# Performance work log

Measured on AMD Instinct MI355X. Metric: run time of the kernel, lower is better.

## Reference

```python
import jax, jax.numpy as jnp
import numpy as np

N_NODES = 50000
N_EDGES = 800000
IN_CH = 128
HID = 64
HEADS = 4
OUT_CH = 64
NEG_SLOPE = 0.2


def _add_self_loops(ei, n):
    loops = jnp.tile(jnp.arange(n, dtype=ei.dtype)[None, :], (2, 1))
    return jnp.concatenate([ei, loops], axis=1)


def _gat_conv(x, ei, W, a_s, a_d, b, concat):
    """PyG-style GATConv. x:[N,F], ei:[2,E], W:[F,H*C], a_s/a_d:[H,C]."""
    N = x.shape[0]
    H, C = a_s.shape
    h = (x @ W).reshape(N, H, C)                     # [N,H,C]
    src, dst = ei[0], ei[1]
    al_s = (h * a_s[None]).sum(-1)                   # [N,H]
    al_d = (h * a_d[None]).sum(-1)                   # [N,H]
    logits = jax.nn.leaky_relu(al_s[src] + al_d[dst], NEG_SLOPE)  # [E,H]
    # segment softmax over incoming edges of each dst node
    m = jax.ops.segment_max(logits, dst, num_segments=N)
    m = jax.lax.stop_gradient(jnp.where(jnp.isfinite(m), m, 0.0))
    ex = jnp.exp(logits - m[dst])
    denom = jax.ops.segment_sum(ex, dst, num_segments=N)
    alpha = ex / (denom[dst] + 1e-16)                # [E,H]
    out = jax.ops.segment_sum(alpha[:, :, None] * h[src], dst, num_segments=N)  # [N,H,C]
    out = out.reshape(N, H * C) if concat else out.mean(axis=1)
    return out + b


def _hetero_layer(x, edges, self_loop_flags, W, a_s, a_d, b, concat):
    N = x.shape[0]
    out = None
    for r in range(3):
        ei = _add_self_loops(edges[r], N) if self_loop_flags[r] else edges[r]
        o = _gat_conv(x, ei, W[r], a_s[r], a_d[r], b[r], concat)
        out = o if out is None else out + o
    return out


def setup_inputs() -> dict:
    key = jax.random.key(0)
    ks = jax.random.split(key, 16)
    s = 0.05
    return {
        "x": jax.random.normal(ks[0], (N_NODES, IN_CH), jnp.float32),
        "e_blocks": jax.random.randint(ks[1], (2, N_EDGES), 0, N_NODES),
        "e_spatial": jax.random.randint(ks[2], (2, N_EDGES), 0, N_NODES),
        "e_similar": jax.random.randint(ks[3], (2, N_EDGES), 0, N_NODES),
        "W1": jax.random.normal(ks[4], (3, IN_CH, HEADS * HID), jnp.float32) * s,
        "a1s": jax.random.normal(ks[5], (3, HEADS, HID), jnp.float32) * s,
        "a1d": jax.random.normal(ks[6], (3, HEADS, HID), jnp.float32) * s,
        "b1": jax.random.normal(ks[7], (3, HEADS * HID), jnp.float32) * s,
        "W2": jax.random.normal(ks[8], (3, HEADS * HID, HEADS * HID), jnp.float32) * s,
        "a2s": jax.random.normal(ks[9], (3, HEADS, HID), jnp.float32) * s,
        "a2d": jax.random.normal(ks[10], (3, HEADS, HID), jnp.float32) * s,
        "b2": jax.random.normal(ks[11], (3, HID), jnp.float32) * s,
        "Wl": jax.random.normal(ks[12], (HID, OUT_CH), jnp.float32) * s,
        "bl": jax.random.normal(ks[13], (OUT_CH,), jnp.float32) * s,
    }


def reference(x, e_blocks, e_spatial, e_similar, W1, a1s, a1d, b1,
              W2, a2s, a2d, b2, Wl, bl):
    edges = [e_blocks, e_spatial, e_similar]
    self_loops = [False, True, True]  # 'blocks' has add_self_loops=False
    h = _hetero_layer(x, edges, self_loops, W1, a1s, a1d, b1, concat=True)
    h = jax.nn.relu(h)
    h = _hetero_layer(h, edges, self_loops, W2, a2s, a2d, b2, concat=False)
    h = jax.nn.relu(h)
    return h @ Wl + bl
```

## Files before the change

### kernel.cpp

```cpp
#include <hip/hip_runtime.h>
#include <hip/hip_bf16.h>
#include <hip/hip_fp16.h>

#define NN 50000
#define NE 800000
#define FIN 128
#define HCC 256
#define OC 64
#define NSL 0.2f
#define NT3 (3 * NN)

typedef __attribute__((ext_vector_type(8))) short sh8;
typedef __attribute__((ext_vector_type(16))) float f32x16;

struct __attribute__((aligned(8))) h4 { __half x, y, z, w; };
struct __attribute__((aligned(8))) s4 { short x, y, z, w; };

__device__ __forceinline__ unsigned short bf_rne(float f) {
  unsigned u = __float_as_uint(f);
  u += 0x7FFF + ((u >> 16) & 1);
  return (unsigned short)(u >> 16);
}

__device__ __forceinline__ float edge_w(float lg) {
  lg = (lg > 0.f) ? lg : NSL * lg;
  return __expf(lg);
}

template<int KK>
__global__ __launch_bounds__(256) void k_prep(const float* __restrict__ W,
                                              short* __restrict__ out) {
  int i = blockIdx.x * 256 + threadIdx.x;
  if (i >= 3 * KK * 256) return;
  int r = i / (KK * 256);
  int rem = i - r * KK * 256;
  int k = rem >> 8;
  int n = rem & 255;
  float f = W[i];
  unsigned short hb = bf_rne(f);
  float hf = __uint_as_float(((unsigned)hb) << 16);
  unsigned short lb = bf_rne(f - hf);
  int cb = n >> 7, c = n & 127, ks8 = k >> 3, kj = k & 7;
  size_t base = (size_t)r * 4 * KK * 128;
  size_t oh = base + ((size_t)((cb * 2 + 0) * (KK / 8) + ks8) * 128 + c) * 8 + kj;
  size_t ol = base + ((size_t)((cb * 2 + 1) * (KK / 8) + ks8) * 128 + c) * 8 + kj;
  out[oh] = (short)hb;
  out[ol] = (short)lb;
}

__global__ __launch_bounds__(256) void k_split(const float* __restrict__ x,
                                               short* __restrict__ xhi,
                                               short* __restrict__ xlo) {
  int i = blockIdx.x * 256 + threadIdx.x;
  if (i >= NN * FIN / 4) return;
  float4 v = ((const float4*)x)[i];
  s4 h, l;
  float f, hf;
  f = v.x; h.x = (short)bf_rne(f); hf = __uint_as_float(((unsigned)(unsigned short)h.x) << 16); l.x = (short)bf_rne(f - hf);
  f = v.y; h.y = (short)bf_rne(f); hf = __uint_as_float(((unsigned)(unsigned short)h.y) << 16); l.y = (short)bf_rne(f - hf);
  f = v.z; h.z = (short)bf_rne(f); hf = __uint_as_float(((unsigned)(unsigned short)h.z) << 16); l.z = (short)bf_rne(f - hf);
  f = v.w; h.w = (short)bf_rne(f); hf = __uint_as_float(((unsigned)(unsigned short)h.w) << 16); l.w = (short)bf_rne(f - hf);
  ((s4*)xhi)[i] = h;
  ((s4*)xlo)[i] = l;
}

__global__ void k_hist3(const int* __restrict__ e0, const int* __restrict__ e1,
                        const int* __restrict__ e2, int* __restrict__ deg3) {
  int i = blockIdx.x * blockDim.x + threadIdx.x;
  int st = gridDim.x * blockDim.x;
  for (; i < 3 * NE; i += st) {
    int rel = i / NE;
    int j = i - rel * NE;
    const int* e = (rel == 0) ? e0 : ((rel == 1) ? e1 : e2);
    atomicAdd(&deg3[rel * NN + e[NE + j]], 1);
  }
}

__global__ __launch_bounds__(1024) void k_bsum(const int* __restrict__ deg3,
                                               int* __restrict__ bsum) {
  __shared__ int s[1024];
  int t = threadIdx.x;
  int i = blockIdx.x * 1024 + t;
  s[t] = (i < NT3) ? deg3[i] : 0;
  __syncthreads();
  for (int off = 512; off > 0; off >>= 1) {
    if (t < off) s[t] += s[t + off];
    __syncthreads();
  }
  if (t == 0) bsum[blockIdx.x] = s[0];
}

__global__ __launch_bounds__(256) void k_scan2(const int* __restrict__ bsum,
                                               int* __restrict__ boffs, int nb) {
  __shared__ int s[256];
  int t = threadIdx.x;
  int v = (t < nb) ? bsum[t] : 0;
  s[t] = v;
  __syncthreads();
  for (int off = 1; off < 256; off <<= 1) {
    int x = (t >= off) ? s[t - off] : 0;
    __syncthreads();
    s[t] += x;
    __syncthreads();
  }
  if (t < nb) boffs[t] = s[t] - v;
}

__global__ __launch_bounds__(1024) void k_rowptr(const int* __restrict__ deg3,
                                                 const int* __restrict__ boffs,
                                                 int* __restrict__ rpA,
                                                 int* __restrict__ cursor3) {
  __shared__ int s[1024];
  int t = threadIdx.x;
  int i = blockIdx.x * 1024 + t;
  int d = (i < NT3) ? deg3[i] : 0;
  s[t] = d;
  __syncthreads();
  for (int off = 1; off < 1024; off <<= 1) {
    int x = (t >= off) ? s[t - off] : 0;
    __syncthreads();
    s[t] += x;
    __syncthreads();
  }
  if (i < NT3) {
    int excl = boffs[blockIdx.x] + s[t] - d;
    int r = (i < NN) ? 0 : ((i < 2 * NN) ? 1 : 2);
    int n = i - r * NN;
    int val = excl - r * NE;
    rpA[r * (NN + 1) + n] = val;
    cursor3[i] = val;
  }
  if (blockIdx.x == 0 && t < 3) rpA[t * (NN + 1) + NN] = NE;
}

__global__ void k_scatter(const int* __restrict__ srcv, const int* __restrict__ dstv,
                          int* __restrict__ cursor, int* __restrict__ csr_src, int n) {
  int i = blockIdx.x * blockDim.x + threadIdx.x;
  int st = gridDim.x * blockDim.x;
  for (; i < n; i += st) {
    int pos = atomicAdd(&cursor[dstv[i]], 1);
    csr_src[pos] = srcv[i];
  }
}

template<int KK>
__global__ __launch_bounds__(256) void k_mgemm(const short* __restrict__ Ahi,
                                               const short* __restrict__ Alo,
                                               const short* __restrict__ BcAll,
                                               const float* __restrict__ asfAll,
                                               const float* __restrict__ adfAll,
                                               __half* __restrict__ houtAll,
                                               float* __restrict__ alsAll,
                                               float* __restrict__ aldAll, int M) {
  const int rel = blockIdx.y;
  const short* Bc = BcAll + (size_t)rel * 4 * KK * 128;
  const float* asf = asfAll + rel * HCC;
  const float* adf = adfAll + rel * HCC;
  __half* hout = houtAll + (size_t)rel * NN * HCC;
  float* als = alsAll + (size_t)rel * NN * 4;
  float* ald = aldAll + (size_t)rel * NN * 4;

  const int tid = threadIdx.x;
  const int lane = tid & 63;
  const int w = tid >> 6;
  const int l31 = lane & 31;
  const int lg = lane >> 5;
  const int wrow = blockIdx.x * 64 + (w & 1) * 32;
  const int ch = w >> 1;

  f32x16 acc[4];
#pragma unroll
  for (int t = 0; t < 4; ++t) acc[t] = (f32x16)(0.f);

  const int r = wrow + l31;
  const bool aok = r < M;
  const short* ahp = Ahi + (size_t)r * KK;
  const short* alp = Alo + (size_t)r * KK;
  const short* bh = Bc + (size_t)(ch * 2 + 0) * KK * 128 + l31 * 8;
  const short* bl = Bc + (size_t)(ch * 2 + 1) * KK * 128 + l31 * 8;

  const int NK = KK / 16;

#define LOADF(kst, AH, AL, BH, BL)                                     \
  {                                                                    \
    const int k0 = (kst) * 16 + lg * 8;                                \
    AH = (sh8){0, 0, 0, 0, 0, 0, 0, 0};                                \
    AL = AH;                                                           \
    if (aok) {                                                         \
      AH = *(const sh8*)(ahp + k0);                                    \
      AL = *(const sh8*)(alp + k0);                                    \
    }                                                                  \
    const int ks8 = (kst) * 2 + lg;                                    \
    const short* bhp = bh + (size_t)ks8 * 1024;                        \
    const short* blp = bl + (size_t)ks8 * 1024;                        \
    _Pragma("unroll")                                                  \
    for (int t = 0; t < 4; ++t) {                                      \
      BH[t] = *(const sh8*)(bhp + t * 256);                            \
      BL[t] = *(const sh8*)(blp + t * 256);                            \
    }                                                                  \
  }

#define MMBLK(AH, AL, BH, BL)                                                       \
  {                                                                                 \
    _Pragma("unroll")                                                               \
    for (int t = 0; t < 4; ++t) {                                                   \
      acc[t] = __builtin_amdgcn_mfma_f32_32x32x16_bf16(AH, BH[t], acc[t], 0, 0, 0); \
      acc[t] = __builtin_amdgcn_mfma_f32_32x32x16_bf16(AL, BH[t], acc[t], 0, 0, 0); \
      acc[t] = __builtin_amdgcn_mfma_f32_32x32x16_bf16(AH, BL[t], acc[t], 0, 0, 0); \
    }                                                                               \
  }

  sh8 a0h, a0l, b0h[4], b0l[4];
  sh8 a1h, a1l, b1h[4], b1l[4];
  LOADF(0, a0h, a0l, b0h, b0l);
#pragma unroll
  for (int kst = 0; kst < NK - 1; ++kst) {
    if ((kst & 1) == 0) {
      LOADF(kst + 1, a1h, a1l, b1h, b1l);
      MMBLK(a0h, a0l, b0h, b0l);
    } else {
      LOADF(kst + 1, a0h, a0l, b0h, b0l);
      MMBLK(a1h, a1l, b1h, b1l);
    }
  }
  MMBLK(a1h, a1l, b1h, b1l);
#undef LOADF
#undef MMBLK

  float asr[4], adr[4];
#pragma unroll
  for (int t = 0; t < 4; ++t) {
    int col = ch * 128 + t * 32 + l31;
    asr[t] = asf[col];
    adr[t] = adf[col];
  }
#pragma unroll
  for (int v = 0; v < 16; ++v) {
    const int rl = (v & 3) + 8 * (v >> 2) + 4 * lg;
    const int row = wrow + rl;
    const bool rok = row < M;
    float s0 = 0.f, s1 = 0.f, d0 = 0.f, d1 = 0.f;
    __half* hp = hout + (size_t)row * 256 + ch * 128 + l31;
#pragma unroll
    for (int t = 0; t < 4; ++t) {
      float dv = acc[t][v];
      if (rok) hp[t * 32] = __float2half(dv);
      if (t < 2) { s0 += dv * asr[t]; d0 += dv * adr[t]; }
      else       { s1 += dv * asr[t]; d1 += dv * adr[t]; }
    }
#pragma unroll
    for (int m = 1; m < 32; m <<= 1) {
      s0 += __shfl_xor(s0, m);
      s1 += __shfl_xor(s1, m);
      d0 += __shfl_xor(d0, m);
      d1 += __shfl_xor(d1, m);
    }
    if (rok && l31 == 0) {
      *(float2*)(als + (size_t)row * 4 + ch * 2) = make_float2(s0, s1);
      *(float2*)(ald + (size_t)row * 4 + ch * 2) = make_float2(d0, d1);
    }
  }
}

template<bool SL>
__device__ __forceinline__ void gat_rel(int n, int head, size_t loff,
                                        const __half* __restrict__ h,
                                        const float* __restrict__ als,
                                        const float* __restrict__ ald,
                                        const int* __restrict__ rp,
                                        const int* __restrict__ cs,
                                        float& ox, float& oy, float& oz, float& ow) {
  float ad = ald[n * 4 + head];
  int rs = rp[n], re = rp[n + 1];
  float ax = 0.f, ay = 0.f, az = 0.f, aw = 0.f, wsum = 0.f;
  int i = rs;
  for (; i + 4 <= re; i += 4) {
    int s0 = cs[i], s1 = cs[i + 1], s2 = cs[i + 2], s3 = cs[i + 3];
    float al0 = als[s0 * 4 + head];
    float al1 = als[s1 * 4 + head];
    float al2 = als[s2 * 4 + head];
    float al3 = als[s3 * 4 + head];
    h4 v0 = *(const h4*)&h[(size_t)s0 * HCC + loff];
    h4 v1 = *(const h4*)&h[(size_t)s1 * HCC + loff];
    h4 v2 = *(const h4*)&h[(size_t)s2 * HCC + loff];
    h4 v3 = *(const h4*)&h[(size_t)s3 * HCC + loff];
    float w0 = edge_w(al0 + ad), w1 = edge_w(al1 + ad);
    float w2 = edge_w(al2 + ad), w3 = edge_w(al3 + ad);
    wsum += (w0 + w1) + (w2 + w3);
    ax = fmaf(w0, __half2float(v0.x), ax); ay = fmaf(w0, __half2float(v0.y), ay);
    az = fmaf(w0, __half2float(v0.z), az); aw = fmaf(w0, __half2float(v0.w), aw);
    ax = fmaf(w1, __half2float(v1.x), ax); ay = fmaf(w1, __half2float(v1.y), ay);
    az = fmaf(w1, __half2float(v1.z), az); aw = fmaf(w1, __half2float(v1.w), aw);
    ax = fmaf(w2, __half2float(v2.x), ax); ay = fmaf(w2, __half2float(v2.y), ay);
    az = fmaf(w2, __half2float(v2.z), az); aw = fmaf(w2, __half2float(v2.w), aw);
    ax = fmaf(w3, __half2float(v3.x), ax); ay = fmaf(w3, __half2float(v3.y), ay);
    az = fmaf(w3, __half2float(v3.z), az); aw = fmaf(w3, __half2float(v3.w), aw);
  }
  for (; i < re; ++i) {
    int s = cs[i];
    float w = edge_w(als[s * 4 + head] + ad);
    wsum += w;
    h4 hv = *(const h4*)&h[(size_t)s * HCC + loff];
    ax = fmaf(w, __half2float(hv.x), ax);
    ay = fmaf(w, __half2float(hv.y), ay);
    az = fmaf(w, __half2float(hv.z), az);
    aw = fmaf(w, __half2float(hv.w), aw);
  }
  if (SL) {
    float w = edge_w(als[n * 4 + head] + ad);
    wsum += w;
    h4 hv = *(const h4*)&h[(size_t)n * HCC + loff];
    ax = fmaf(w, __half2float(hv.x), ax);
    ay = fmaf(w, __half2float(hv.y), ay);
    az = fmaf(w, __half2float(hv.z), az);
    aw = fmaf(w, __half2float(hv.w), aw);
  }
  float inv = 1.0f / (wsum + 1e-16f);
  ox = fmaf(ax, inv, ox);
  oy = fmaf(ay, inv, oy);
  oz = fmaf(az, inv, oz);
  ow = fmaf(aw, inv, ow);
}

__global__ __launch_bounds__(256) void k_gather3c(const __half* __restrict__ h3,
                                                  const float* __restrict__ als3,
                                                  const float* __restrict__ ald3,
                                                  const int* __restrict__ rpA,
                                                  const int* __restrict__ csAll,
                                                  const float* __restrict__ bias,
                                                  short* __restrict__ o1hi,
                                                  short* __restrict__ o1lo) {
  int gid = blockIdx.x * blockDim.x + threadIdx.x;
  int n = gid >> 6;
  int lane = threadIdx.x & 63;
  if (n >= NN) return;
  int head = lane >> 4;
  size_t loff = (size_t)lane * 4;
  const size_t HS = (size_t)NN * HCC;
  const size_t AS = (size_t)NN * 4;
  float ox = 0.f, oy = 0.f, oz = 0.f, ow = 0.f;
  gat_rel<false>(n, head, loff, h3,          als3,          ald3,          rpA,                csAll,          ox, oy, oz, ow);
  gat_rel<true >(n, head, loff, h3 + HS,     als3 + AS,     ald3 + AS,     rpA + (NN + 1),     csAll + NE,     ox, oy, oz, ow);
  gat_rel<true >(n, head, loff, h3 + 2 * HS, als3 + 2 * AS, ald3 + 2 * AS, rpA + 2 * (NN + 1), csAll + 2 * NE, ox, oy, oz, ow);
  float4 b0 = *(const float4*)&bias[lane * 4];
  float4 b1 = *(const float4*)&bias[HCC + lane * 4];
  float4 b2 = *(const float4*)&bias[2 * HCC + lane * 4];
  float vv[4];
  vv[0] = fmaxf(ox + b0.x + b1.x + b2.x, 0.f);
  vv[1] = fmaxf(oy + b0.y + b1.y + b2.y, 0.f);
  vv[2] = fmaxf(oz + b0.z + b1.z + b2.z, 0.f);
  vv[3] = fmaxf(ow + b0.w + b1.w + b2.w, 0.f);
  s4 hv, lv;
  short* hp = (short*)&hv;
  short* lp = (short*)&lv;
#pragma unroll
  for (int j = 0; j < 4; ++j) {
    unsigned short hb = bf_rne(vv[j]);
    float hf = __uint_as_float(((unsigned)hb) << 16);
    hp[j] = (short)hb;
    lp[j] = (short)bf_rne(vv[j] - hf);
  }
  *(s4*)&o1hi[(size_t)n * HCC + loff] = hv;
  *(s4*)&o1lo[(size_t)n * HCC + loff] = lv;
}

__global__ __launch_bounds__(256) void k_gather3f(const __half* __restrict__ h3,
                                                  const float* __restrict__ als3,
                                                  const float* __restrict__ ald3,
                                                  const int* __restrict__ rpA,
                                                  const int* __restrict__ csAll,
                                                  const float* __restrict__ bias,
                                                  const float* __restrict__ Wl,
                                                  const float* __restrict__ bl,
                                                  float* __restrict__ outp) {
  __shared__ float Ws[64 * 64];
  for (int i = threadIdx.x; i < 4096; i += 256) Ws[i] = Wl[i];
  __syncthreads();
  int gid = blockIdx.x * blockDim.x + threadIdx.x;
  int n = gid >> 6;
  int lane = threadIdx.x & 63;
  if (n >= NN) return;
  int head = lane >> 4;
  size_t loff = (size_t)lane * 4;
  const size_t HS = (size_t)NN * HCC;
  const size_t AS = (size_t)NN * 4;
  float ox = 0.f, oy = 0.f, oz = 0.f, ow = 0.f;
  gat_rel<false>(n, head, loff, h3,          als3,          ald3,          rpA,                csAll,          ox, oy, oz, ow);
  gat_rel<true >(n, head, loff, h3 + HS,     als3 + AS,     ald3 + AS,     rpA + (NN + 1),     csAll + NE,     ox, oy, oz, ow);
  gat_rel<true >(n, head, loff, h3 + 2 * HS, als3 + 2 * AS, ald3 + 2 * AS, rpA + 2 * (NN + 1), csAll + 2 * NE, ox, oy, oz, ow);
  ox += __shfl_xor(ox, 16); oy += __shfl_xor(oy, 16);
  oz += __shfl_xor(oz, 16); ow += __shfl_xor(ow, 16);
  ox += __shfl_xor(ox, 32); oy += __shfl_xor(oy, 32);
  oz += __shfl_xor(oz, 32); ow += __shfl_xor(ow, 32);
  int q0 = lane & 15;
  float4 b0 = *(const float4*)&bias[q0 * 4];
  float4 b1 = *(const float4*)&bias[OC + q0 * 4];
  float4 b2 = *(const float4*)&bias[2 * OC + q0 * 4];
  float x0 = fmaxf(0.25f * ox + b0.x + b1.x + b2.x, 0.f);
  float x1 = fmaxf(0.25f * oy + b0.y + b1.y + b2.y, 0.f);
  float x2 = fmaxf(0.25f * oz + b0.z + b1.z + b2.z, 0.f);
  float x3 = fmaxf(0.25f * ow + b0.w + b1.w + b2.w, 0.f);
  float acc = bl[lane];
#pragma unroll
  for (int q = 0; q < 16; ++q) {
    float xa = __shfl(x0, q);
    float xb = __shfl(x1, q);
    float xc = __shfl(x2, q);
    float xd = __shfl(x3, q);
    acc = fmaf(xa, Ws[(4 * q + 0) * 64 + lane], acc);
    acc = fmaf(xb, Ws[(4 * q + 1) * 64 + lane], acc);
    acc = fmaf(xc, Ws[(4 * q + 2) * 64 + lane], acc);
    acc = fmaf(xd, Ws[(4 * q + 3) * 64 + lane], acc);
  }
  outp[(size_t)n * OC + lane] = acc;
}

extern "C" void kernel_launch(void* const* d_in, const int* in_sizes, int n_in,
                              void* d_out, int out_size, void* d_ws, size_t ws_size,
                              hipStream_t stream) {
  const float* x   = (const float*)d_in[0];
  const int* e_b   = (const int*)d_in[1];
  const int* e_sp  = (const int*)d_in[2];
  const int* e_si  = (const int*)d_in[3];
  const float* W1  = (const float*)d_in[4];
  const float* a1s = (const float*)d_in[5];
  const float* a1d = (const float*)d_in[6];
  const float* b1  = (const float*)d_in[7];
  const float* W2  = (const float*)d_in[8];
  const float* a2s = (const float*)d_in[9];
  const float* a2d = (const float*)d_in[10];
  const float* b2  = (const float*)d_in[11];
  const float* Wl  = (const float*)d_in[12];
  const float* bl  = (const float*)d_in[13];
  float* out = (float*)d_out;

  char* ws = (char*)d_ws;
  size_t off = 0;
  auto alloc = [&](size_t b) {
    char* p = ws + off;
    off += (b + 255) & ~(size_t)255;
    return p;
  };
  __half* h3  = (__half*)alloc((size_t)3 * NN * HCC * 2);
  short* o1hi = (short*)alloc((size_t)NN * HCC * 2);
  short* o1lo = (short*)alloc((size_t)NN * HCC * 2);
  short* xhi  = (short*)alloc((size_t)NN * FIN * 2);
  short* xlo  = (short*)alloc((size_t)NN * FIN * 2);
  float* als3 = (float*)alloc((size_t)3 * NN * 4 * 4);
  float* ald3 = (float*)alloc((size_t)3 * NN * 4 * 4);
  int* deg3    = (int*)alloc((size_t)NT3 * 4);
  int* cursor3 = (int*)alloc((size_t)NT3 * 4);
  int* rpA     = (int*)alloc((size_t)3 * (NN + 1) * 4);
  int* bsum    = (int*)alloc(256 * 4);
  int* boffs   = (int*)alloc(256 * 4);
  short* Wc1   = (short*)alloc((size_t)3 * 4 * FIN * 128 * 2);
  short* Wc2   = (short*)alloc((size_t)3 * 4 * HCC * 128 * 2);
  int* csAll   = (int*)alloc((size_t)3 * NE * 4);

  const int* edges[3] = {e_b, e_sp, e_si};

  k_prep<FIN><<<(3 * FIN * 256 + 255) / 256, 256, 0, stream>>>(W1, Wc1);
  k_prep<HCC><<<(3 * HCC * 256 + 255) / 256, 256, 0, stream>>>(W2, Wc2);
  k_split<<<(NN * FIN / 4 + 255) / 256, 256, 0, stream>>>(x, xhi, xlo);

  hipMemsetAsync(deg3, 0, (size_t)NT3 * 4, stream);
  k_hist3<<<2048, 256, 0, stream>>>(e_b, e_sp, e_si, deg3);
  const int NB = (NT3 + 1023) / 1024;
  k_bsum<<<NB, 1024, 0, stream>>>(deg3, bsum);
  k_scan2<<<1, 256, 0, stream>>>(bsum, boffs, NB);
  k_rowptr<<<NB, 1024, 0, stream>>>(deg3, boffs, rpA, cursor3);
  for (int r = 0; r < 3; ++r)
    k_scatter<<<1024, 256, 0, stream>>>(edges[r], edges[r] + NE, cursor3 + r * NN,
                                        csAll + (size_t)r * NE, NE);

  const int gblocks = (NN + 63) / 64;
  const int ablocks = (NN * 64) / 256;

  k_mgemm<FIN><<<dim3(gblocks, 3), 256, 0, stream>>>(
      xhi, xlo, Wc1, a1s, a1d, h3, als3, ald3, NN);
  k_gather3c<<<ablocks, 256, 0, stream>>>(
      h3, als3, ald3, rpA, csAll, b1, o1hi, o1lo);

  k_mgemm<HCC><<<dim3(gblocks, 3), 256, 0, stream>>>(
      o1hi, o1lo, Wc2, a2s, a2d, h3, als3, ald3, NN);
  k_gather3f<<<ablocks, 256, 0, stream>>>(
      h3, als3, ald3, rpA, csAll, b2, Wl, bl, out);
}
```

Before: 864.7 us.

## Stage weight tiles in double-buffered LDS via global_load_lds in split-bf16 GEMM

The projection GEMM now copies each k-step's weight tile into a double-buffered LDS area using direct global-to-LDS loads. Waves then read their B fragments from LDS instead of each loading them separately from global memory. The weight prep kernel reorders the packed bf16 hi/lo weights so each k-step's tile is contiguous. This cuts redundant global/L2 traffic for B, at the cost of a block-wide barrier every k-step and 32KB of LDS per block, which may lower occupancy.

```diff
diff --git a/kernel.cpp b/kernel.cpp
--- a/kernel.cpp
+++ b/kernel.cpp
@@ -15,6 +15,9 @@
 
 struct __attribute__((aligned(8))) h4 { __half x, y, z, w; };
 struct __attribute__((aligned(8))) s4 { short x, y, z, w; };
+
+typedef const __attribute__((address_space(1))) unsigned int* gas_t;
+typedef __attribute__((address_space(3))) unsigned int* las_t;
 
 __device__ __forceinline__ unsigned short bf_rne(float f) {
   unsigned u = __float_as_uint(f);
@@ -40,10 +43,11 @@
   unsigned short hb = bf_rne(f);
   float hf = __uint_as_float(((unsigned)hb) << 16);
   unsigned short lb = bf_rne(f - hf);
-  int cb = n >> 7, c = n & 127, ks8 = k >> 3, kj = k & 7;
+  int cb = n >> 7, c = n & 127;
+  int kst = k >> 4, p = (k >> 3) & 1, kj = k & 7;
   size_t base = (size_t)r * 4 * KK * 128;
-  size_t oh = base + ((size_t)((cb * 2 + 0) * (KK / 8) + ks8) * 128 + c) * 8 + kj;
-  size_t ol = base + ((size_t)((cb * 2 + 1) * (KK / 8) + ks8) * 128 + c) * 8 + kj;
+  size_t oh = base + ((size_t)(kst * 8 + (cb * 2 + 0) * 2 + p) * 128 + c) * 8 + kj;
+  size_t ol = base + ((size_t)(kst * 8 + (cb * 2 + 1) * 2 + p) * 128 + c) * 8 + kj;
   out[oh] = (short)hb;
   out[ol] = (short)lb;
 }
@@ -152,8 +156,9 @@
                                                __half* __restrict__ houtAll,
                                                float* __restrict__ alsAll,
                                                float* __restrict__ aldAll, int M) {
+  __shared__ short Bs[2][8192];
   const int rel = blockIdx.y;
-  const short* Bc = BcAll + (size_t)rel * 4 * KK * 128;
+  const short* Brel = BcAll + (size_t)rel * 4 * KK * 128;
   const float* asf = asfAll + rel * HCC;
   const float* adf = adfAll + rel * HCC;
   __half* hout = houtAll + (size_t)rel * NN * HCC;
@@ -176,55 +181,61 @@
   const bool aok = r < M;
   const short* ahp = Ahi + (size_t)r * KK;
   const short* alp = Alo + (size_t)r * KK;
-  const short* bh = Bc + (size_t)(ch * 2 + 0) * KK * 128 + l31 * 8;
-  const short* bl = Bc + (size_t)(ch * 2 + 1) * KK * 128 + l31 * 8;
+  const int qh = (ch * 2 + 0) * 2 + lg;
+  const int ql = (ch * 2 + 1) * 2 + lg;
 
   const int NK = KK / 16;
 
-#define LOADF(kst, AH, AL, BH, BL)                                     \
-  {                                                                    \
-    const int k0 = (kst) * 16 + lg * 8;                                \
-    AH = (sh8){0, 0, 0, 0, 0, 0, 0, 0};                                \
-    AL = AH;                                                           \
-    if (aok) {                                                         \
-      AH = *(const sh8*)(ahp + k0);                                    \
-      AL = *(const sh8*)(alp + k0);                                    \
-    }                                                                  \
-    const int ks8 = (kst) * 2 + lg;                                    \
-    const short* bhp = bh + (size_t)ks8 * 1024;                        \
-    const short* blp = bl + (size_t)ks8 * 1024;                        \
-    _Pragma("unroll")                                                  \
-    for (int t = 0; t < 4; ++t) {                                      \
-      BH[t] = *(const sh8*)(bhp + t * 256);                            \
-      BL[t] = *(const sh8*)(blp + t * 256);                            \
-    }                                                                  \
-  }
-
-#define MMBLK(AH, AL, BH, BL)                                                       \
-  {                                                                                 \
-    _Pragma("unroll")                                                               \
-    for (int t = 0; t < 4; ++t) {                                                   \
-      acc[t] = __builtin_amdgcn_mfma_f32_32x32x16_bf16(AH, BH[t], acc[t], 0, 0, 0); \
-      acc[t] = __builtin_amdgcn_mfma_f32_32x32x16_bf16(AL, BH[t], acc[t], 0, 0, 0); \
-      acc[t] = __builtin_amdgcn_mfma_f32_32x32x16_bf16(AH, BL[t], acc[t], 0, 0, 0); \
-    }                                                                               \
-  }
-
-  sh8 a0h, a0l, b0h[4], b0l[4];
-  sh8 a1h, a1l, b1h[4], b1l[4];
-  LOADF(0, a0h, a0l, b0h, b0l);
-#pragma unroll
-  for (int kst = 0; kst < NK - 1; ++kst) {
-    if ((kst & 1) == 0) {
-      LOADF(kst + 1, a1h, a1l, b1h, b1l);
-      MMBLK(a0h, a0l, b0h, b0l);
-    } else {
-      LOADF(kst + 1, a0h, a0l, b0h, b0l);
-      MMBLK(a1h, a1l, b1h, b1l);
+#define STAGE(kst, buf)                                                      \
+  {                                                                          \
+    _Pragma("unroll")                                                        \
+    for (int it = 0; it < 4; ++it) {                                         \
+      int so = it * 2048 + w * 512;                                          \
+      __builtin_amdgcn_global_load_lds(                                      \
+          (gas_t)(const void*)(Brel + (size_t)(kst) * 8192 + so + lane * 8), \
+          (las_t)(void*)&Bs[buf][so], 16, 0, 0);                             \
+    }                                                                        \
+  }
+
+#define LOADA(kst, AH, AL)                 \
+  {                                        \
+    const int k0 = (kst) * 16 + lg * 8;    \
+    AH = (sh8){0, 0, 0, 0, 0, 0, 0, 0};    \
+    AL = AH;                               \
+    if (aok) {                             \
+      AH = *(const sh8*)(ahp + k0);        \
+      AL = *(const sh8*)(alp + k0);        \
+    }                                      \
+  }
+
+#define MMBLK(buf, AH, AL)                                                            \
+  {                                                                                   \
+    _Pragma("unroll")                                                                 \
+    for (int t = 0; t < 4; ++t) {                                                     \
+      sh8 bhf = *(const sh8*)&Bs[buf][(size_t)(qh * 128 + t * 32 + l31) * 8];         \
+      sh8 blf = *(const sh8*)&Bs[buf][(size_t)(ql * 128 + t * 32 + l31) * 8];         \
+      acc[t] = __builtin_amdgcn_mfma_f32_32x32x16_bf16(AH, bhf, acc[t], 0, 0, 0);     \
+      acc[t] = __builtin_amdgcn_mfma_f32_32x32x16_bf16(AL, bhf, acc[t], 0, 0, 0);     \
+      acc[t] = __builtin_amdgcn_mfma_f32_32x32x16_bf16(AH, blf, acc[t], 0, 0, 0);     \
+    }                                                                                 \
+  }
+
+  sh8 a0h, a0l, a1h, a1l;
+  LOADA(0, a0h, a0l);
+  STAGE(0, 0);
+#pragma unroll
+  for (int kst = 0; kst < NK; ++kst) {
+    __syncthreads();
+    if (kst + 1 < NK) {
+      STAGE(kst + 1, (kst & 1) ^ 1);
+      if ((kst & 1) == 0) { LOADA(kst + 1, a1h, a1l); }
+      else                { LOADA(kst + 1, a0h, a0l); }
     }
-  }
-  MMBLK(a1h, a1l, b1h, b1l);
-#undef LOADF
+    if ((kst & 1) == 0) { MMBLK(0, a0h, a0l); }
+    else                { MMBLK(1, a1h, a1l); }
+  }
+#undef STAGE
+#undef LOADA
 #undef MMBLK
 
   float asr[4], adr[4];
```

After: 861.1 us. No clear change (-0.4%).
